# Optimization experiments

Measured on AMD Instinct MI355X. Metric: run time of the kernel, lower is better.

The kernel has to match this reference:

```python
import jax, jax.numpy as jnp
import numpy as np

B, N, DIN, DOUT = 8, 2048, 128, 128

def setup_inputs() -> dict:
    key = jax.random.key(0)
    k1, k2, k3, k4 = jax.random.split(key, 4)
    x = jax.random.normal(k1, (B, N, DIN), dtype=jnp.float32)
    adj = jax.random.uniform(k2, (B, N, N), dtype=jnp.float32)
    W = jax.random.normal(k3, (DIN, DOUT), dtype=jnp.float32) / np.sqrt(DIN)
    b = jax.random.normal(k4, (DOUT,), dtype=jnp.float32) * 0.01
    return {"x": x, "adj": adj, "W": W, "b": b}

def reference(x, adj, W, b):
    # degree over last dim of adj: [B, N]
    degree = jnp.sum(adj, axis=2)
    d_norm = 1.0 / jnp.sqrt(degree + 1e-8)
    # D^{-1/2} A D^{-1/2} == row/col elementwise scaling (same math as diag_embed+bmm)
    adj_norm = d_norm[:, :, None] * adj * d_norm[:, None, :]
    support = jnp.einsum('bnm,bmd->bnd', adj_norm, x)  # [B, N, DIN]
    return support @ W + b  # [B, N, DOUT]
```

## Files before the change

kernel.cpp:

```cpp
#include <hip/hip_runtime.h>
#include <hip/hip_bf16.h>

#define NN 2048
#define DD 128

typedef __attribute__((ext_vector_type(4))) float f32x4;
typedef __attribute__((ext_vector_type(8))) short short8;

__device__ __forceinline__ unsigned short f2bf_bits(float f) {
  union { __hip_bfloat16 h; unsigned short s; } u;
  u.h = __float2bfloat16(f);
  return u.s;
}

__device__ __forceinline__ short8 cvt8(f32x4 a, f32x4 b) {
  short8 r;
  r[0] = (short)f2bf_bits(a[0]); r[1] = (short)f2bf_bits(a[1]);
  r[2] = (short)f2bf_bits(a[2]); r[3] = (short)f2bf_bits(a[3]);
  r[4] = (short)f2bf_bits(b[0]); r[5] = (short)f2bf_bits(b[1]);
  r[6] = (short)f2bf_bits(b[2]); r[7] = (short)f2bf_bits(b[3]);
  return r;
}

__device__ __forceinline__ void gld16(const void* src, void* lds) {
  __builtin_amdgcn_global_load_lds(
      (const __attribute__((address_space(1))) void*)src,
      (__attribute__((address_space(3))) void*)lds, 16, 0, 0);
}

__global__ void k_degree(const float* __restrict__ adj, float* __restrict__ dnorm) {
  const int wv = threadIdx.x >> 6;
  const int ln = threadIdx.x & 63;
  const int row = blockIdx.x * 4 + wv;
  const f32x4* rowp = (const f32x4*)(adj + (size_t)row * NN);
  float s = 0.0f;
#pragma unroll
  for (int i = 0; i < 8; ++i) {
    f32x4 v = rowp[i * 64 + ln];
    s += v[0] + v[1] + v[2] + v[3];
  }
#pragma unroll
  for (int off = 32; off >= 1; off >>= 1) s += __shfl_xor(s, off);
  if (ln == 0) dnorm[row] = rsqrtf(s + 1e-8f);
}

__global__ void k_y(const float* __restrict__ x, const float* __restrict__ W,
                    const float* __restrict__ dnorm, short* __restrict__ yT) {
  const int ln = threadIdx.x & 63;
  const int wv = threadIdx.x >> 6;
  const int bb = blockIdx.x >> 5;
  const int n0 = (blockIdx.x & 31) << 6;
  const int l15 = ln & 15, l4 = ln >> 4;
  const int dbase = wv * 32;

  short8 af[2][4];
#pragma unroll
  for (int dt = 0; dt < 2; ++dt)
#pragma unroll
    for (int ks = 0; ks < 4; ++ks) {
      short8 a;
#pragma unroll
      for (int j = 0; j < 8; ++j)
        a[j] = (short)f2bf_bits(W[(size_t)(ks * 32 + l4 * 8 + j) * DD + dbase + dt * 16 + l15]);
      af[dt][ks] = a;
    }

  f32x4 acc[2][4];
#pragma unroll
  for (int dt = 0; dt < 2; ++dt)
#pragma unroll
    for (int nt = 0; nt < 4; ++nt) acc[dt][nt] = (f32x4)0.0f;

  const float* xb = x + (size_t)bb * NN * DD;
  const float* dnb = dnorm + (size_t)bb * NN;
#pragma unroll
  for (int nt = 0; nt < 4; ++nt) {
    const int n = n0 + nt * 16 + l15;
    const float dn = dnb[n];
#pragma unroll
    for (int ks = 0; ks < 4; ++ks) {
      f32x4 p = *(const f32x4*)(xb + (size_t)n * DD + ks * 32 + l4 * 8);
      f32x4 q = *(const f32x4*)(xb + (size_t)n * DD + ks * 32 + l4 * 8 + 4);
      short8 bf = cvt8(p * dn, q * dn);
#pragma unroll
      for (int dt = 0; dt < 2; ++dt)
        acc[dt][nt] = __builtin_amdgcn_mfma_f32_16x16x32_bf16(af[dt][ks], bf, acc[dt][nt], 0, 0, 0);
    }
  }

  short* yb = yT + (size_t)bb * DD * NN;
#pragma unroll
  for (int dt = 0; dt < 2; ++dt)
#pragma unroll
    for (int nt = 0; nt < 4; ++nt)
#pragma unroll
      for (int rr = 0; rr < 4; ++rr) {
        int d = dbase + dt * 16 + l4 * 4 + rr;
        yb[(size_t)d * NN + n0 + nt * 16 + l15] = (short)f2bf_bits(acc[dt][nt][rr]);
      }
}

__launch_bounds__(512, 1)
__global__ void k_gemm2(const float* __restrict__ adj, const short* __restrict__ yT,
                        const float* __restrict__ dnorm, const float* __restrict__ bias,
                        float* __restrict__ out) {
  __shared__ float As[4][4096];

  const int t = threadIdx.x;
  const int ln = t & 63;
  const int wv = t >> 6;
  const int orig = ((blockIdx.x & 7) << 5) | (blockIdx.x >> 3);
  const int bb = orig >> 5;
  const int m0 = (orig & 31) << 6;

  const char* ablk = (const char*)(adj + ((size_t)bb * NN + m0) * NN);
  const int oc = (wv << 4) + (ln & 15);
  const int kg8 = (ln >> 4) << 3;
  const short* ybase = yT + ((size_t)bb * DD + oc) * NN;

  f32x4 acc[4];
#pragma unroll
  for (int m = 0; m < 4; ++m) acc[m] = (f32x4)0.0f;

  auto stage = [&](int tile, int buf) {
#pragma unroll
    for (int j = 0; j < 2; ++j) {
      unsigned L = ((unsigned)j << 13) + ((unsigned)t << 4);
      unsigned row = L >> 8;
      unsigned off = L & 255u;
      unsigned soff = off ^ ((row & 7u) << 4);
      const char* src = ablk + (size_t)row * (NN * 4) + (size_t)tile * 256 + soff;
      gld16(src, (char*)As + buf * 16384 + L);
    }
  };
  auto loadB = [&](int tile, int ks) -> short8 {
    return *(const short8*)(ybase + (tile << 6) + ks * 32 + kg8);
  };
  auto compute = [&](int buf, short8 b0, short8 b1) {
    const char* base = (const char*)As + buf * 16384;
#pragma unroll
    for (int ks = 0; ks < 2; ++ks) {
      short8 bf = ks ? b1 : b0;
#pragma unroll
      for (int m = 0; m < 4; ++m) {
        unsigned row = (unsigned)(m * 16 + (ln & 15));
        unsigned c = (unsigned)(ks * 128 + (ln >> 4) * 32);
        unsigned sw = (row & 7u) << 4;
        f32x4 f0 = *(const f32x4*)(base + (row << 8) + (c ^ sw));
        f32x4 f1 = *(const f32x4*)(base + (row << 8) + ((c + 16) ^ sw));
        acc[m] = __builtin_amdgcn_mfma_f32_16x16x32_bf16(cvt8(f0, f1), bf, acc[m], 0, 0, 0);
      }
    }
  };

  stage(0, 0); stage(1, 1); stage(2, 2);
  short8 p0k0 = loadB(0, 0), p0k1 = loadB(0, 1);
  short8 p1k0 = loadB(1, 0), p1k1 = loadB(1, 1);
  short8 p2k0 = loadB(2, 0), p2k1 = loadB(2, 1);
  short8 p3k0 = loadB(3, 0), p3k1 = loadB(3, 1);
  asm volatile("s_waitcnt vmcnt(0)\n\ts_barrier" ::: "memory");

#define GITER(T, PK0, PK1)                                              \
  {                                                                     \
    stage(((T) + 3) & 31, ((T) + 3) & 3);                               \
    short8 nb0 = loadB(((T) + 4) & 31, 0);                              \
    short8 nb1 = loadB(((T) + 4) & 31, 1);                              \
    compute((T) & 3, PK0, PK1);                                         \
    asm volatile("s_waitcnt vmcnt(10)\n\ts_barrier" ::: "memory");      \
    PK0 = nb0; PK1 = nb1;                                               \
  }

#pragma unroll 1
  for (int t4 = 0; t4 < 32; t4 += 4) {
    GITER(t4 + 0, p0k0, p0k1);
    GITER(t4 + 1, p1k0, p1k1);
    GITER(t4 + 2, p2k0, p2k1);
    GITER(t4 + 3, p3k0, p3k1);
  }
#undef GITER

  const float bv = bias[oc];
  const int rbase = (ln >> 4) << 2;
#pragma unroll
  for (int m = 0; m < 4; ++m) {
    f32x4 dn = *(const f32x4*)(dnorm + (size_t)bb * NN + m0 + m * 16 + rbase);
#pragma unroll
    for (int rr = 0; rr < 4; ++rr)
      out[(size_t)(bb * NN + m0 + m * 16 + rbase + rr) * DD + oc] = acc[m][rr] * dn[rr] + bv;
  }
}

extern "C" void kernel_launch(void* const* d_in, const int* in_sizes, int n_in,
                              void* d_out, int out_size, void* d_ws, size_t ws_size,
                              hipStream_t stream) {
  (void)in_sizes; (void)n_in; (void)out_size; (void)ws_size;
  const float* x = (const float*)d_in[0];
  const float* adj = (const float*)d_in[1];
  const float* W = (const float*)d_in[2];
  const float* bias = (const float*)d_in[3];
  float* out = (float*)d_out;

  char* ws = (char*)d_ws;
  float* dnorm = (float*)ws;
  short* yT = (short*)(ws + (1 << 16));

  k_degree<<<4096, 256, 0, stream>>>(adj, dnorm);
  k_y<<<256, 256, 0, stream>>>(x, W, dnorm, yT);
  k_gemm2<<<256, 512, 0, stream>>>(adj, yT, dnorm, bias, out);
}
```

Baseline: 69.68 us.

## Switch adjacency GEMM to 32x32x16 MFMA with 2x4 wave tiling

The main aggregation GEMM now gives each wave a 32x32 output tile (2 row slabs × 4 column quarters) computed with the 32x32x16 bf16 MFMA, replacing the 16-column by 64-row tiles that used 16x16x32 MFMAs. Each wave reads only its own 32 rows of the adjacency tile from LDS instead of all 64, which halves LDS reads and fp32-to-bf16 conversions per wave. The B-operand prefetch is restructured into two ping-pong register sets loaded after compute, with the wait count adjusted to match. In exchange the B prefetch is now only two tiles deep and is issued after compute, so global latency may be less well hidden.

```diff
diff --git a/kernel.cpp b/kernel.cpp
--- a/kernel.cpp
+++ b/kernel.cpp
@@ -5,6 +5,7 @@
 #define DD 128
 
 typedef __attribute__((ext_vector_type(4))) float f32x4;
+typedef __attribute__((ext_vector_type(16))) float f32x16;
 typedef __attribute__((ext_vector_type(8))) short short8;
 
 __device__ __forceinline__ unsigned short f2bf_bits(float f) {
@@ -101,7 +102,7 @@
 }
 
 __launch_bounds__(512, 1)
-__global__ void k_gemm2(const float* __restrict__ adj, const short* __restrict__ yT,
+__global__ void k_gemm6(const float* __restrict__ adj, const short* __restrict__ yT,
                         const float* __restrict__ dnorm, const float* __restrict__ bias,
                         float* __restrict__ out) {
   __shared__ float As[4][4096];
@@ -109,18 +110,18 @@
   const int t = threadIdx.x;
   const int ln = t & 63;
   const int wv = t >> 6;
+  const int l31 = ln & 31, lhi = ln >> 5;
+  const int ms = wv >> 2;
+  const int dq = wv & 3;
   const int orig = ((blockIdx.x & 7) << 5) | (blockIdx.x >> 3);
   const int bb = orig >> 5;
   const int m0 = (orig & 31) << 6;
 
   const char* ablk = (const char*)(adj + ((size_t)bb * NN + m0) * NN);
-  const int oc = (wv << 4) + (ln & 15);
-  const int kg8 = (ln >> 4) << 3;
-  const short* ybase = yT + ((size_t)bb * DD + oc) * NN;
-
-  f32x4 acc[4];
-#pragma unroll
-  for (int m = 0; m < 4; ++m) acc[m] = (f32x4)0.0f;
+  const int col = (dq << 5) + l31;
+  const short* ybase = yT + ((size_t)bb * DD + col) * NN + (lhi << 3);
+
+  f32x16 acc = (f32x16)0.0f;
 
   auto stage = [&](int tile, int buf) {
 #pragma unroll
@@ -133,60 +134,56 @@
       gld16(src, (char*)As + buf * 16384 + L);
     }
   };
-  auto loadB = [&](int tile, int ks) -> short8 {
-    return *(const short8*)(ybase + (tile << 6) + ks * 32 + kg8);
+  auto loadB = [&](int tile, short8 B[4]) {
+#pragma unroll
+    for (int ksp = 0; ksp < 4; ++ksp)
+      B[ksp] = *(const short8*)(ybase + (tile << 6) + ksp * 16);
   };
-  auto compute = [&](int buf, short8 b0, short8 b1) {
+  auto compute = [&](int buf, short8 B[4]) {
     const char* base = (const char*)As + buf * 16384;
-#pragma unroll
-    for (int ks = 0; ks < 2; ++ks) {
-      short8 bf = ks ? b1 : b0;
-#pragma unroll
-      for (int m = 0; m < 4; ++m) {
-        unsigned row = (unsigned)(m * 16 + (ln & 15));
-        unsigned c = (unsigned)(ks * 128 + (ln >> 4) * 32);
-        unsigned sw = (row & 7u) << 4;
-        f32x4 f0 = *(const f32x4*)(base + (row << 8) + (c ^ sw));
-        f32x4 f1 = *(const f32x4*)(base + (row << 8) + ((c + 16) ^ sw));
-        acc[m] = __builtin_amdgcn_mfma_f32_16x16x32_bf16(cvt8(f0, f1), bf, acc[m], 0, 0, 0);
-      }
+    const unsigned row = (unsigned)((ms << 5) + l31);
+    const unsigned sw = (row & 7u) << 4;
+    const char* rbase = base + (row << 8);
+    const unsigned kh = (unsigned)lhi << 5;
+#pragma unroll
+    for (int ksp = 0; ksp < 4; ++ksp) {
+      unsigned c = (unsigned)(ksp * 64) + kh;
+      f32x4 f0 = *(const f32x4*)(rbase + (c ^ sw));
+      f32x4 f1 = *(const f32x4*)(rbase + ((c + 16) ^ sw));
+      acc = __builtin_amdgcn_mfma_f32_32x32x16_bf16(cvt8(f0, f1), B[ksp], acc, 0, 0, 0);
     }
   };
 
+  short8 E[4], O[4];
   stage(0, 0); stage(1, 1); stage(2, 2);
-  short8 p0k0 = loadB(0, 0), p0k1 = loadB(0, 1);
-  short8 p1k0 = loadB(1, 0), p1k1 = loadB(1, 1);
-  short8 p2k0 = loadB(2, 0), p2k1 = loadB(2, 1);
-  short8 p3k0 = loadB(3, 0), p3k1 = loadB(3, 1);
+  loadB(0, E); loadB(1, O);
   asm volatile("s_waitcnt vmcnt(0)\n\ts_barrier" ::: "memory");
 
-#define GITER(T, PK0, PK1)                                              \
+#define GITER(T, BSLOT)                                                 \
   {                                                                     \
     stage(((T) + 3) & 31, ((T) + 3) & 3);                               \
-    short8 nb0 = loadB(((T) + 4) & 31, 0);                              \
-    short8 nb1 = loadB(((T) + 4) & 31, 1);                              \
-    compute((T) & 3, PK0, PK1);                                         \
-    asm volatile("s_waitcnt vmcnt(10)\n\ts_barrier" ::: "memory");      \
-    PK0 = nb0; PK1 = nb1;                                               \
+    compute((T) & 3, BSLOT);                                            \
+    loadB(((T) + 2) & 31, BSLOT);                                       \
+    asm volatile("s_waitcnt vmcnt(16)\n\ts_barrier" ::: "memory");      \
   }
 
 #pragma unroll 1
-  for (int t4 = 0; t4 < 32; t4 += 4) {
-    GITER(t4 + 0, p0k0, p0k1);
-    GITER(t4 + 1, p1k0, p1k1);
-    GITER(t4 + 2, p2k0, p2k1);
-    GITER(t4 + 3, p3k0, p3k1);
+  for (int t2 = 0; t2 < 32; t2 += 2) {
+    GITER(t2 + 0, E);
+    GITER(t2 + 1, O);
   }
 #undef GITER
 
-  const float bv = bias[oc];
-  const int rbase = (ln >> 4) << 2;
-#pragma unroll
-  for (int m = 0; m < 4; ++m) {
-    f32x4 dn = *(const f32x4*)(dnorm + (size_t)bb * NN + m0 + m * 16 + rbase);
-#pragma unroll
-    for (int rr = 0; rr < 4; ++rr)
-      out[(size_t)(bb * NN + m0 + m * 16 + rbase + rr) * DD + oc] = acc[m][rr] * dn[rr] + bv;
+  const float bv = bias[col];
+  const int rowbase = m0 + (ms << 5) + (lhi << 2);
+#pragma unroll
+  for (int q = 0; q < 4; ++q) {
+    f32x4 dn4 = *(const f32x4*)(dnorm + (size_t)bb * NN + rowbase + 8 * q);
+#pragma unroll
+    for (int j = 0; j < 4; ++j) {
+      const int row = rowbase + 8 * q + j;
+      out[((size_t)bb * NN + row) * DD + col] = acc[q * 4 + j] * dn4[j] + bv;
+    }
   }
 }
 
@@ -206,5 +203,5 @@
 
   k_degree<<<4096, 256, 0, stream>>>(adj, dnorm);
   k_y<<<256, 256, 0, stream>>>(x, W, dnorm, yT);
-  k_gemm2<<<256, 512, 0, stream>>>(adj, yT, dnorm, bias, out);
-}
+  k_gemm6<<<256, 512, 0, stream>>>(adj, yT, dnorm, bias, out);
+}
```

Measured after the change: 75.94 us. 1.09x slower.
